# Optimization experiments

Measured on AMD Instinct MI355X. Metric: run time of the kernel, lower is better.

Reference implementation:

```python
import jax, jax.numpy as jnp
import numpy as np

B, N, C, HF, NUM_CLASS = 2, 500, 512, 25, 20
POOL = 7
STRIDE = 32.0


def setup_inputs() -> dict:
    key = jax.random.key(0)
    ks = jax.random.split(key, 9)
    feature_map = jax.random.normal(ks[0], (B, C, HF, HF), dtype=jnp.float32)
    # Post-NMS boxes (r0, c0, r1, c1) in image coords [0, 800], guaranteed
    # to have floor(r1/32) - floor(r0/32) >= 1 so every crop is non-empty
    # (matches the module's assumption that extract_fature_map is non-empty).
    r0 = jax.random.uniform(ks[1], (B, N), minval=0.0, maxval=700.0)
    c0 = jax.random.uniform(ks[2], (B, N), minval=0.0, maxval=700.0)
    hh = jax.random.uniform(ks[3], (B, N), minval=64.0, maxval=100.0)
    ww = jax.random.uniform(ks[4], (B, N), minval=64.0, maxval=100.0)
    boxes = jnp.stack([r0, c0, jnp.clip(r0 + hh, 0, 800.0), jnp.clip(c0 + ww, 0, 800.0)], axis=-1)
    fc_w = jax.random.normal(ks[5], (4096, POOL * POOL * C), dtype=jnp.float32) * 0.01
    fc_b = jnp.zeros((4096,), dtype=jnp.float32)
    l_w = jax.random.normal(ks[6], (NUM_CLASS * 4, 4096), dtype=jnp.float32) * 0.01
    l_b = jnp.zeros((NUM_CLASS * 4,), dtype=jnp.float32)
    s_w = jax.random.normal(ks[7], (NUM_CLASS + 1, 4096), dtype=jnp.float32) * 0.01
    s_b = jnp.zeros((NUM_CLASS + 1,), dtype=jnp.float32)
    return {"feature_map": feature_map, "boxes": boxes, "fc_w": fc_w, "fc_b": fc_b,
            "l_w": l_w, "l_b": l_b, "s_w": s_w, "s_b": s_b}


def _bin_edges(start, size):
    # Adaptive avg pool bin boundaries: floor(k*size/P), ceil((k+1)*size/P),
    # offset by the crop start. start/size: [B, N] int32. Returns [B, N, P] each.
    k = jnp.arange(POOL, dtype=jnp.int32)
    lo = start[..., None] + (k * size[..., None]) // POOL
    hi = start[..., None] + ((k + 1) * size[..., None] + POOL - 1) // POOL
    return lo, hi


def _roi_pool(feature_map, boxes):
    # Exact equivalent of per-box crop + AdaptiveAvgPool2d((7,7)) via an
    # integral image, fully vectorized over all B*N boxes.
    coords = (boxes / STRIDE).astype(jnp.int32)  # int() cast, coords >= 0
    r0, c0, r1, c1 = coords[..., 0], coords[..., 1], coords[..., 2], coords[..., 3]
    rs, re = _bin_edges(r0, r1 - r0)  # [B, N, 7]
    cs, ce = _bin_edges(c0, c1 - c0)
    # Integral image: I[b, ch, i, j] = sum(fm[b, ch, :i, :j]); shape [B, C, 26, 26]
    I = jnp.pad(feature_map, ((0, 0), (0, 0), (1, 0), (1, 0))).cumsum(2).cumsum(3)

    def pool_one(I_b, rs_b, re_b, cs_b, ce_b):
        def corner(r, c):  # [N,7],[N,7] -> [C, N, 7, 7]
            return I_b[:, r[:, :, None], c[:, None, :]]
        S = corner(re_b, ce_b) - corner(rs_b, ce_b) - corner(re_b, cs_b) + corner(rs_b, cs_b)
        area = ((re_b - rs_b)[:, :, None] * (ce_b - cs_b)[:, None, :]).astype(I_b.dtype)
        return S / area  # [C, N, 7, 7]

    pooled = jax.vmap(pool_one)(I, rs, re, cs, ce)  # [B, C, N, 7, 7]
    # torch.flatten(pool, 0) flattens (C, 7, 7) in C-major order
    return pooled.transpose(0, 2, 1, 3, 4).reshape(B, N, C * POOL * POOL)


def reference(feature_map, boxes, fc_w, fc_b, l_w, l_b, s_w, s_b):
    feat = _roi_pool(feature_map, boxes)                      # [B, N, 25088]
    fc = jnp.einsum('bnk,fk->bnf', feat, fc_w) + fc_b         # [B, N, 4096]
    l_fc = jnp.einsum('bnf,lf->bnl', fc, l_w) + l_b           # [B, N, 80]
    s_fc = jnp.einsum('bnf,sf->bns', fc, s_w) + s_b           # [B, N, 21]
    max_index = jnp.argmax(s_fc, axis=-1)                     # [B, N]
    idx = max_index[..., None] + jnp.arange(4)                # l_fc[mi:mi+4]
    l_out = jnp.take_along_axis(l_fc, idx, axis=-1)           # [B, N, 4]
    return l_out, s_fc
```

## Files before the change

### kernel.cpp

```cpp
#include <hip/hip_runtime.h>

#define BATCH 2
#define NBOX 500
#define CH 512
#define HFD 25
#define IW 26
#define IRC 676
#define IRCP2 768
#define PPOOL 7
#define NP 49
#define NCLS 20
#define NO 101
#define OP2 112
#define MFRAG 7
#define KD 25088
#define FDIM 4096
#define NSTEP_TOT 128
#define FSPLIT 8
#define WCSTEPS 16
#define S_WC ((size_t)KD * OP2)
#define NFRAG_H (NP * 16 * MFRAG)

typedef __attribute__((ext_vector_type(4))) float f32x4;
typedef __attribute__((ext_vector_type(8))) short bf16x8;
typedef __attribute__((ext_vector_type(4))) unsigned int u32v4;

#define MFMA16 __builtin_amdgcn_mfma_f32_16x16x32_bf16

typedef __attribute__((address_space(1))) const unsigned int guint;
typedef __attribute__((address_space(3))) unsigned int luint;
#define GLL16(G, L) __builtin_amdgcn_global_load_lds((guint*)(G), (luint*)(L), 16, 0, 0)

#define SPLIT2PK(V0, V1, HW, MW)                                       \
  {                                                                    \
    unsigned u0_ = __float_as_uint(V0), u1_ = __float_as_uint(V1);     \
    HW = (u0_ >> 16) | (u1_ & 0xffff0000u);                            \
    float r0_ = (V0) - __uint_as_float(u0_ & 0xffff0000u);             \
    float r1_ = (V1) - __uint_as_float(u1_ & 0xffff0000u);             \
    unsigned m0_ = __float_as_uint(r0_), m1_ = __float_as_uint(r1_);   \
    m0_ += 0x7fffu + ((m0_ >> 16) & 1u);                               \
    m1_ += 0x7fffu + ((m1_ >> 16) & 1u);                               \
    MW = (m0_ >> 16) | (m1_ & 0xffff0000u);                            \
  }

#define SPLIT2T(V0, V1, HW, MW)                                        \
  {                                                                    \
    unsigned u0_ = __float_as_uint(V0), u1_ = __float_as_uint(V1);     \
    HW = (u0_ >> 16) | (u1_ & 0xffff0000u);                            \
    float r0_ = (V0) - __uint_as_float(u0_ & 0xffff0000u);             \
    float r1_ = (V1) - __uint_as_float(u1_ & 0xffff0000u);             \
    MW = (__float_as_uint(r0_) >> 16) |                                \
         (__float_as_uint(r1_) & 0xffff0000u);                         \
  }

#define SPLIT3PK(V0, V1, HW, MW, LW)                                   \
  {                                                                    \
    unsigned u0_ = __float_as_uint(V0), u1_ = __float_as_uint(V1);     \
    HW = (u0_ >> 16) | (u1_ & 0xffff0000u);                            \
    float r0_ = (V0) - __uint_as_float(u0_ & 0xffff0000u);             \
    float r1_ = (V1) - __uint_as_float(u1_ & 0xffff0000u);             \
    unsigned m0_ = __float_as_uint(r0_), m1_ = __float_as_uint(r1_);   \
    MW = (m0_ >> 16) | (m1_ & 0xffff0000u);                            \
    float s0_ = r0_ - __uint_as_float(m0_ & 0xffff0000u);              \
    float s1_ = r1_ - __uint_as_float(m1_ & 0xffff0000u);              \
    LW = (__float_as_uint(s0_) >> 16) |                                \
         (__float_as_uint(s1_) & 0xffff0000u);                         \
  }

__global__ void k_lt(const float* __restrict__ lw, const float* __restrict__ sw,
                     u32v4* __restrict__ Ahi, u32v4* __restrict__ Amd) {
    int t = blockIdx.x * 256 + threadIdx.x;
    if (t >= MFRAG * NSTEP_TOT * 64) return;
    int lane = t & 63;
    int wv = t >> 6;
    int s = wv & 127, mf = wv >> 7;
    int o = mf * 16 + (lane & 15);
    int f0 = s * 32 + (lane >> 4) * 8;
    float v[8];
    const float* row = nullptr;
    if (o < 80) row = lw + (size_t)o * FDIM;
    else if (o < NO) row = sw + (size_t)(o - 80) * FDIM;
    #pragma unroll
    for (int j = 0; j < 8; ++j) v[j] = row ? row[f0 + j] : 0.f;
    u32v4 hw, mw;
    #pragma unroll
    for (int w = 0; w < 4; ++w)
        SPLIT2PK(v[2 * w], v[2 * w + 1], hw[w], mw[w]);
    Ahi[(size_t)wv * 64 + lane] = hw;
    Amd[(size_t)wv * 64 + lane] = mw;
}

__global__ void k_integral(const float* __restrict__ fm, float* __restrict__ I) {
    int gtid = blockIdx.x * blockDim.x + threadIdx.x;
    int wid = gtid >> 6;
    int lane = gtid & 63;
    if (wid >= BATCH * CH) return;
    const float* src = fm + (size_t)wid * (HFD * HFD);
    float* dst = I + (size_t)wid * IRCP2;
    if (lane < IW) dst[lane] = 0.f;
    if (lane >= 1 && lane < IW) dst[lane * IW] = 0.f;
    int c = lane;
    float acc = 0.f;
    for (int r = 0; r < HFD; ++r) {
        float v = (c < HFD) ? src[r * HFD + c] : 0.f;
        #pragma unroll
        for (int d = 1; d < 32; d <<= 1) {
            float t = __shfl_up(v, d, 64);
            if (lane >= d) v += t;
        }
        acc += v;
        if (c < HFD) dst[(r + 1) * IW + (c + 1)] = acc;
    }
}

__global__ void k_bias(const float* __restrict__ lw, const float* __restrict__ sw,
                       const float* __restrict__ fcb, const float* __restrict__ lb,
                       const float* __restrict__ sb, float* __restrict__ bias) {
    int o = blockIdx.x;
    __shared__ float red[256];
    float s = 0.f;
    if (o < NO) {
        const float* row = (o < 80) ? (lw + (size_t)o * FDIM) : (sw + (size_t)(o - 80) * FDIM);
        for (int f = threadIdx.x; f < FDIM; f += 256) s += row[f] * fcb[f];
    }
    red[threadIdx.x] = s;
    __syncthreads();
    for (int st = 128; st > 0; st >>= 1) {
        if ((int)threadIdx.x < st) red[threadIdx.x] += red[threadIdx.x + st];
        __syncthreads();
    }
    if (threadIdx.x == 0) {
        float bv = 0.f;
        if (o < 80) bv = red[0] + lb[o];
        else if (o < NO) bv = red[0] + sb[o - 80];
        bias[o] = bv;
    }
}

#define WC_STAGE(S, DB)                                                       \
  {                                                                           \
    const float* gb_ = W1 + (size_t)(fs * 512 + (S) * 32 + w) * KD + k0;      \
    _Pragma("unroll")                                                         \
    for (int i_ = 0; i_ < 8; ++i_) {                                          \
      unsigned gc_ = (lb16 ^ ((unsigned)(i_ >> 1) << 6)) >> 2;                \
      GLL16(gb_ + (size_t)(4 * i_) * KD + gc_,                                \
            &Bs[DB][i_ * 1024 + w * 256]);                                    \
    }                                                                         \
  }

#define WC_STEP(S, DB)                                                        \
  {                                                                           \
    u32v4 ah[MFRAG], am[MFRAG];                                               \
    _Pragma("unroll")                                                         \
    for (int mf = 0; mf < MFRAG; ++mf) {                                      \
      size_t ai = (size_t)((mf * 128 + fs * WCSTEPS + (S)) * 64 + lane);      \
      ah[mf] = Ahi[ai]; am[mf] = Amd[ai];                                     \
    }                                                                         \
    const char* bs_ = (const char*)&Bs[DB][0];                                \
    _Pragma("unroll")                                                         \
    for (int nf = 0; nf < 4; ++nf) {                                          \
      float bv[8];                                                            \
      _Pragma("unroll")                                                       \
      for (int j = 0; j < 8; ++j)                                             \
        bv[j] = *(const float*)(bs_ + (rowg * 8 + j) * 1024 + kb[nf]);        \
      u32v4 bhw, bmw;                                                         \
      _Pragma("unroll")                                                       \
      for (int w_ = 0; w_ < 4; ++w_)                                          \
        SPLIT2T(bv[2 * w_], bv[2 * w_ + 1], bhw[w_], bmw[w_]);                \
      bf16x8 bh = __builtin_bit_cast(bf16x8, bhw);                            \
      bf16x8 bm = __builtin_bit_cast(bf16x8, bmw);                            \
      _Pragma("unroll")                                                       \
      for (int mf = 0; mf < MFRAG; ++mf) {                                    \
        bf16x8 a_h = __builtin_bit_cast(bf16x8, ah[mf]);                      \
        bf16x8 a_m = __builtin_bit_cast(bf16x8, am[mf]);                      \
        acc[mf][nf] = MFMA16(a_h, bh, acc[mf][nf], 0, 0, 0);                  \
        acc[mf][nf] = MFMA16(a_m, bh, acc[mf][nf], 0, 0, 0);                  \
        acc[mf][nf] = MFMA16(a_h, bm, acc[mf][nf], 0, 0, 0);                  \
      }                                                                       \
    }                                                                         \
  }

__global__ void __launch_bounds__(256, 2) k_wc(const float* __restrict__ W1,
                                               const u32v4* __restrict__ Ahi,
                                               const u32v4* __restrict__ Amd,
                                               float* __restrict__ Wcp) {
    __shared__ float Bs[2][32 * 256];
    int lane = threadIdx.x & 63;
    int w = threadIdx.x >> 6;
    int kblk = blockIdx.x;
    int fs = blockIdx.y;
    int k0 = kblk * 256;
    int col = lane & 15, rowg = lane >> 4;
    unsigned lb16 = (unsigned)lane * 16;

    unsigned kb[4];
    #pragma unroll
    for (int nf = 0; nf < 4; ++nf)
        kb[nf] = ((unsigned)((w * 64 + nf * 16 + col) * 4)) ^ ((unsigned)rowg << 6);

    f32x4 acc[MFRAG][4];
    #pragma unroll
    for (int mf = 0; mf < MFRAG; ++mf)
        #pragma unroll
        for (int nf = 0; nf < 4; ++nf)
            acc[mf][nf] = (f32x4){0.f, 0.f, 0.f, 0.f};

    WC_STAGE(0, 0);
    __syncthreads();
    for (int s = 0; s < WCSTEPS; ++s) {
        int db = s & 1;
        if (s + 1 < WCSTEPS) WC_STAGE(s + 1, db ^ 1);
        WC_STEP(s, db);
        __syncthreads();
    }

    float* wp = Wcp + (size_t)fs * S_WC;
    #pragma unroll
    for (int mf = 0; mf < MFRAG; ++mf)
        #pragma unroll
        for (int nf = 0; nf < 4; ++nf) {
            size_t k = (size_t)k0 + w * 64 + nf * 16 + col;
            int o = mf * 16 + (rowg << 2);
            *(f32x4*)(wp + k * OP2 + o) = acc[mf][nf];
        }
}

__global__ void k_redsplit(const float* __restrict__ Wcp, u32v4* __restrict__ Whi,
                           u32v4* __restrict__ Wmd, u32v4* __restrict__ Wlo) {
    int t = blockIdx.x * 256 + threadIdx.x;
    int lane = t & 63;
    int fi = t >> 6;
    int p = fi / (16 * MFRAG);
    int rem = fi - p * (16 * MFRAG);
    int cs = rem / MFRAG, mf = rem - cs * MFRAG;
    int o = mf * 16 + (lane & 15);
    int c0 = cs * 32 + (lane >> 4) * 8;
    float v[8];
    #pragma unroll
    for (int j = 0; j < 8; ++j) {
        size_t base = ((size_t)(c0 + j) * NP + p) * OP2 + o;
        float s = 0.f;
        #pragma unroll
        for (int i = 0; i < FSPLIT; ++i) s += Wcp[base + (size_t)i * S_WC];
        v[j] = s;
    }
    u32v4 hw, mw, lww;
    #pragma unroll
    for (int w = 0; w < 4; ++w)
        SPLIT3PK(v[2 * w], v[2 * w + 1], hw[w], mw[w], lww[w]);
    Whi[(size_t)fi * 64 + lane] = hw;
    Wmd[(size_t)fi * 64 + lane] = mw;
    Wlo[(size_t)fi * 64 + lane] = lww;
}

#define KH_STEP(CUR, NXT, S)                                                  \
  {                                                                           \
    if ((S) + 1 < 16) {                                                       \
      _Pragma("unroll")                                                       \
      for (int nf = 0; nf < 2; ++nf)                                          \
        _Pragma("unroll")                                                     \
        for (int j = 0; j < 8; ++j)                                           \
          NXT[nf][j] = Ib[(size_t)(((S) + 1) * 32 + rowg * 8 + j) * IRCP2 + nf * 16]; \
    }                                                                         \
    bf16x8 bh[2], bm[2], bl[2];                                               \
    _Pragma("unroll")                                                         \
    for (int nf = 0; nf < 2; ++nf) {                                          \
      u32v4 bhw, bmw, blw;                                                    \
      _Pragma("unroll")                                                       \
      for (int w_ = 0; w_ < 4; ++w_)                                          \
        SPLIT3PK(CUR[nf][2 * w_], CUR[nf][2 * w_ + 1], bhw[w_], bmw[w_], blw[w_]); \
      bh[nf] = __builtin_bit_cast(bf16x8, bhw);                               \
      bm[nf] = __builtin_bit_cast(bf16x8, bmw);                               \
      bl[nf] = __builtin_bit_cast(bf16x8, blw);                               \
    }                                                                         \
    _Pragma("unroll")                                                         \
    for (int mf = 0; mf < MFRAG; ++mf) {                                      \
      size_t ai = (size_t)(((p * 16 + (S)) * MFRAG + mf) * 64 + lane);        \
      bf16x8 a_h = __builtin_bit_cast(bf16x8, Whi[ai]);                       \
      bf16x8 a_m = __builtin_bit_cast(bf16x8, Wmd[ai]);                       \
      bf16x8 a_l = __builtin_bit_cast(bf16x8, Wlo[ai]);                       \
      _Pragma("unroll")                                                       \
      for (int nf = 0; nf < 2; ++nf) {                                        \
        acc[mf][nf] = MFMA16(a_h, bh[nf], acc[mf][nf], 0, 0, 0);              \
        acc[mf][nf] = MFMA16(a_m, bh[nf], acc[mf][nf], 0, 0, 0);              \
        acc[mf][nf] = MFMA16(a_h, bm[nf], acc[mf][nf], 0, 0, 0);              \
        acc[mf][nf] = MFMA16(a_m, bm[nf], acc[mf][nf], 0, 0, 0);              \
        acc[mf][nf] = MFMA16(a_l, bh[nf], acc[mf][nf], 0, 0, 0);              \
        acc[mf][nf] = MFMA16(a_h, bl[nf], acc[mf][nf], 0, 0, 0);              \
      }                                                                       \
    }                                                                         \
  }

__global__ void __launch_bounds__(256, 2) k_h(const float* __restrict__ I,
                                              const u32v4* __restrict__ Whi,
                                              const u32v4* __restrict__ Wmd,
                                              const u32v4* __restrict__ Wlo,
                                              float* __restrict__ H) {
    int lane = threadIdx.x & 63;
    int w = threadIdx.x >> 6;
    int rcb = blockIdx.x, p = blockIdx.y, b = blockIdx.z;
    int col = lane & 15, rowg = lane >> 4;
    int rcw = rcb * 128 + w * 32;
    const float* Ib = I + (size_t)b * CH * IRCP2 + rcw + col;

    f32x4 acc[MFRAG][2];
    #pragma unroll
    for (int mf = 0; mf < MFRAG; ++mf) {
        acc[mf][0] = (f32x4){0.f, 0.f, 0.f, 0.f};
        acc[mf][1] = (f32x4){0.f, 0.f, 0.f, 0.f};
    }
    float ib0[2][8], ib1[2][8];
    #pragma unroll
    for (int nf = 0; nf < 2; ++nf)
        #pragma unroll
        for (int j = 0; j < 8; ++j)
            ib0[nf][j] = Ib[(size_t)(rowg * 8 + j) * IRCP2 + nf * 16];

    for (int s = 0; s < 16; s += 2) {
        KH_STEP(ib0, ib1, s);
        KH_STEP(ib1, ib0, s + 1);
    }

    #pragma unroll
    for (int mf = 0; mf < MFRAG; ++mf)
        #pragma unroll
        for (int nf = 0; nf < 2; ++nf) {
            int rc = rcw + nf * 16 + col;
            if (rc < IRC) {
                float* hp = H + (((size_t)(b * NP + p)) * IRC + rc) * OP2
                            + mf * 16 + rowg * 4;
                *(f32x4*)hp = acc[mf][nf];
            }
        }
}

__global__ void __launch_bounds__(256) k_out(const float* __restrict__ boxes,
                                             const float* __restrict__ H,
                                             const float* __restrict__ bias,
                                             float* __restrict__ out) {
    int n = blockIdx.x, b = blockIdx.y;
    int t = threadIdx.x;
    __shared__ int srs[PPOOL], sre[PPOOL], scs[PPOOL], sce[PPOOL];
    __shared__ float sinv[NP];
    __shared__ float psum[2][NO];
    __shared__ float sl[NO];
    __shared__ int smi;
    const float* bx = boxes + ((size_t)b * NBOX + n) * 4;
    if (t < PPOOL) {
        int r0 = (int)(bx[0] / 32.0f);
        int c0 = (int)(bx[1] / 32.0f);
        int r1 = (int)(bx[2] / 32.0f);
        int c1 = (int)(bx[3] / 32.0f);
        int sr = r1 - r0, sc = c1 - c0;
        srs[t] = r0 + (t * sr) / PPOOL;
        sre[t] = r0 + ((t + 1) * sr + PPOOL - 1) / PPOOL;
        scs[t] = c0 + (t * sc) / PPOOL;
        sce[t] = c0 + ((t + 1) * sc + PPOOL - 1) / PPOOL;
    }
    __syncthreads();
    if (t < NP) {
        int ph = t / PPOOL, pw = t - ph * PPOOL;
        sinv[t] = 1.0f / (float)((sre[ph] - srs[ph]) * (sce[pw] - scs[pw]));
    }
    __syncthreads();
    int o = t & 127, half = t >> 7;
    if (o < NO) {
        int p0 = half * 25, p1 = half ? NP : 25;
        float acc = 0.f;
        const float* Hb = H + (size_t)b * NP * IRC * OP2 + o;
        for (int p = p0; p < p1; ++p) {
            int ph = p / PPOOL, pw = p - ph * PPOOL;
            const float* Hp = Hb + (size_t)p * IRC * OP2;
            int re = sre[ph], rs = srs[ph], ce = sce[pw], cs = scs[pw];
            float v = Hp[(size_t)(re * IW + ce) * OP2] - Hp[(size_t)(rs * IW + ce) * OP2]
                    - Hp[(size_t)(re * IW + cs) * OP2] + Hp[(size_t)(rs * IW + cs) * OP2];
            acc += v * sinv[p];
        }
        psum[half][o] = acc;
    }
    __syncthreads();
    if (t < NO) {
        float v = psum[0][t] + psum[1][t] + bias[t];
        sl[t] = v;
        if (t >= 80)
            out[(size_t)(4 * BATCH * NBOX) + ((size_t)b * NBOX + n) * (NCLS + 1) + (t - 80)] = v;
    }
    __syncthreads();
    if (t == 0) {
        float best = sl[80]; int mi = 0;
        for (int s = 1; s <= NCLS; ++s) {
            float v = sl[80 + s];
            if (v > best) { best = v; mi = s; }
        }
        smi = mi;
    }
    __syncthreads();
    if (t < 4) out[((size_t)b * NBOX + n) * 4 + t] = sl[smi + t];
}

extern "C" void kernel_launch(void* const* d_in, const int* in_sizes, int n_in,
                              void* d_out, int out_size, void* d_ws, size_t ws_size,
                              hipStream_t stream) {
    const float* fm    = (const float*)d_in[0];
    const float* boxes = (const float*)d_in[1];
    const float* fcw   = (const float*)d_in[2];
    const float* fcb   = (const float*)d_in[3];
    const float* lw    = (const float*)d_in[4];
    const float* lb    = (const float*)d_in[5];
    const float* sw    = (const float*)d_in[6];
    const float* sb    = (const float*)d_in[7];
    float* out = (float*)d_out;

    float* ws = (float*)d_ws;
    float* I    = ws;
    u32v4* Ahi  = (u32v4*)(I + (size_t)BATCH * CH * IRCP2);
    u32v4* Amd  = Ahi + MFRAG * NSTEP_TOT * 64;
    float* bias = (float*)(Amd + MFRAG * NSTEP_TOT * 64);
    float* Wcp  = bias + 128;
    u32v4* Whi  = (u32v4*)(Wcp + (size_t)FSPLIT * S_WC);
    u32v4* Wmd  = Whi + (size_t)NFRAG_H * 64;
    u32v4* Wlo  = Wmd + (size_t)NFRAG_H * 64;
    float* H    = (float*)(Wlo + (size_t)NFRAG_H * 64);

    hipLaunchKernelGGL(k_lt, dim3(224), dim3(256), 0, stream, lw, sw, Ahi, Amd);
    hipLaunchKernelGGL(k_integral, dim3(256), dim3(256), 0, stream, fm, I);
    hipLaunchKernelGGL(k_bias, dim3(104), dim3(256), 0, stream, lw, sw, fcb, lb, sb, bias);
    hipLaunchKernelGGL(k_wc, dim3(98, FSPLIT), dim3(256), 0, stream, fcw, Ahi, Amd, Wcp);
    hipLaunchKernelGGL(k_redsplit, dim3(NFRAG_H * 64 / 256), dim3(256), 0, stream, Wcp, Whi, Wmd, Wlo);
    hipLaunchKernelGGL(k_h, dim3(6, NP, BATCH), dim3(256), 0, stream, I, Whi, Wmd, Wlo, H);
    hipLaunchKernelGGL(k_out, dim3(NBOX, BATCH), dim3(256), 0, stream, boxes, H, bias, out);
}
```

Before: 250.7 us.

## Replace split-K partial buffers with atomic accumulation and widen k_out to four slices

The k_wc split-K partials are now accumulated directly into a single zeroed buffer with float atomics. This replaces writing eight separate partial slabs that k_redsplit then summed, so the partial traffic shrinks from eight slabs to one and the reduction kernel only reads once. The trade is a memset plus contended atomic traffic, and the summation order is no longer deterministic. Separately, k_out now uses 512 threads, splitting the 49 pool bins over four thread groups instead of two to expose more parallel gather loads per box.

```diff
diff --git a/kernel.cpp b/kernel.cpp
--- a/kernel.cpp
+++ b/kernel.cpp
@@ -183,7 +183,7 @@
 __global__ void __launch_bounds__(256, 2) k_wc(const float* __restrict__ W1,
                                                const u32v4* __restrict__ Ahi,
                                                const u32v4* __restrict__ Amd,
-                                               float* __restrict__ Wcp) {
+                                               float* __restrict__ Wc) {
     __shared__ float Bs[2][32 * 256];
     int lane = threadIdx.x & 63;
     int w = threadIdx.x >> 6;
@@ -214,18 +214,19 @@
         __syncthreads();
     }
 
-    float* wp = Wcp + (size_t)fs * S_WC;
     #pragma unroll
     for (int mf = 0; mf < MFRAG; ++mf)
         #pragma unroll
         for (int nf = 0; nf < 4; ++nf) {
             size_t k = (size_t)k0 + w * 64 + nf * 16 + col;
-            int o = mf * 16 + (rowg << 2);
-            *(f32x4*)(wp + k * OP2 + o) = acc[mf][nf];
+            float* dst = Wc + k * OP2 + mf * 16 + (rowg << 2);
+            #pragma unroll
+            for (int j = 0; j < 4; ++j)
+                unsafeAtomicAdd(dst + j, acc[mf][nf][j]);
         }
 }
 
-__global__ void k_redsplit(const float* __restrict__ Wcp, u32v4* __restrict__ Whi,
+__global__ void k_redsplit(const float* __restrict__ Wc, u32v4* __restrict__ Whi,
                            u32v4* __restrict__ Wmd, u32v4* __restrict__ Wlo) {
     int t = blockIdx.x * 256 + threadIdx.x;
     int lane = t & 63;
@@ -237,13 +238,8 @@
     int c0 = cs * 32 + (lane >> 4) * 8;
     float v[8];
     #pragma unroll
-    for (int j = 0; j < 8; ++j) {
-        size_t base = ((size_t)(c0 + j) * NP + p) * OP2 + o;
-        float s = 0.f;
-        #pragma unroll
-        for (int i = 0; i < FSPLIT; ++i) s += Wcp[base + (size_t)i * S_WC];
-        v[j] = s;
-    }
+    for (int j = 0; j < 8; ++j)
+        v[j] = Wc[((size_t)(c0 + j) * NP + p) * OP2 + o];
     u32v4 hw, mw, lww;
     #pragma unroll
     for (int w = 0; w < 4; ++w)
@@ -334,7 +330,7 @@
         }
 }
 
-__global__ void __launch_bounds__(256) k_out(const float* __restrict__ boxes,
+__global__ void __launch_bounds__(512) k_out(const float* __restrict__ boxes,
                                              const float* __restrict__ H,
                                              const float* __restrict__ bias,
                                              float* __restrict__ out) {
@@ -342,7 +338,7 @@
     int t = threadIdx.x;
     __shared__ int srs[PPOOL], sre[PPOOL], scs[PPOOL], sce[PPOOL];
     __shared__ float sinv[NP];
-    __shared__ float psum[2][NO];
+    __shared__ float psum[4][NO];
     __shared__ float sl[NO];
     __shared__ int smi;
     const float* bx = boxes + ((size_t)b * NBOX + n) * 4;
@@ -363,9 +359,10 @@
         sinv[t] = 1.0f / (float)((sre[ph] - srs[ph]) * (sce[pw] - scs[pw]));
     }
     __syncthreads();
-    int o = t & 127, half = t >> 7;
+    int o = t & 127, q = t >> 7;
     if (o < NO) {
-        int p0 = half * 25, p1 = half ? NP : 25;
+        int p0 = q ? (12 * q + 1) : 0;
+        int p1 = 12 * q + 13;
         float acc = 0.f;
         const float* Hb = H + (size_t)b * NP * IRC * OP2 + o;
         for (int p = p0; p < p1; ++p) {
@@ -376,11 +373,11 @@
                     - Hp[(size_t)(re * IW + cs) * OP2] + Hp[(size_t)(rs * IW + cs) * OP2];
             acc += v * sinv[p];
         }
-        psum[half][o] = acc;
+        psum[q][o] = acc;
     }
     __syncthreads();
     if (t < NO) {
-        float v = psum[0][t] + psum[1][t] + bias[t];
+        float v = psum[0][t] + psum[1][t] + psum[2][t] + psum[3][t] + bias[t];
         sl[t] = v;
         if (t >= 80)
             out[(size_t)(4 * BATCH * NBOX) + ((size_t)b * NBOX + n) * (NCLS + 1) + (t - 80)] = v;
@@ -416,17 +413,18 @@
     u32v4* Ahi  = (u32v4*)(I + (size_t)BATCH * CH * IRCP2);
     u32v4* Amd  = Ahi + MFRAG * NSTEP_TOT * 64;
     float* bias = (float*)(Amd + MFRAG * NSTEP_TOT * 64);
-    float* Wcp  = bias + 128;
-    u32v4* Whi  = (u32v4*)(Wcp + (size_t)FSPLIT * S_WC);
+    float* Wc   = bias + 128;
+    u32v4* Whi  = (u32v4*)(Wc + S_WC);
     u32v4* Wmd  = Whi + (size_t)NFRAG_H * 64;
     u32v4* Wlo  = Wmd + (size_t)NFRAG_H * 64;
     float* H    = (float*)(Wlo + (size_t)NFRAG_H * 64);
 
+    hipMemsetAsync(Wc, 0, S_WC * sizeof(float), stream);
     hipLaunchKernelGGL(k_lt, dim3(224), dim3(256), 0, stream, lw, sw, Ahi, Amd);
     hipLaunchKernelGGL(k_integral, dim3(256), dim3(256), 0, stream, fm, I);
     hipLaunchKernelGGL(k_bias, dim3(104), dim3(256), 0, stream, lw, sw, fcb, lb, sb, bias);
-    hipLaunchKernelGGL(k_wc, dim3(98, FSPLIT), dim3(256), 0, stream, fcw, Ahi, Amd, Wcp);
-    hipLaunchKernelGGL(k_redsplit, dim3(NFRAG_H * 64 / 256), dim3(256), 0, stream, Wcp, Whi, Wmd, Wlo);
+    hipLaunchKernelGGL(k_wc, dim3(98, FSPLIT), dim3(256), 0, stream, fcw, Ahi, Amd, Wc);
+    hipLaunchKernelGGL(k_redsplit, dim3(NFRAG_H * 64 / 256), dim3(256), 0, stream, Wc, Whi, Wmd, Wlo);
     hipLaunchKernelGGL(k_h, dim3(6, NP, BATCH), dim3(256), 0, stream, I, Whi, Wmd, Wlo, H);
-    hipLaunchKernelGGL(k_out, dim3(NBOX, BATCH), dim3(256), 0, stream, boxes, H, bias, out);
-}
+    hipLaunchKernelGGL(k_out, dim3(NBOX, BATCH), dim3(512), 0, stream, boxes, H, bias, out);
+}
```

New measurement: 466.7 us. 86.2% more time.
